# Optimization experiments

Measured on AMD Instinct MI355X. Metric: run time of the kernel, lower is better.

The kernel has to match this reference:

```python
import jax, jax.numpy as jnp
import numpy as np
import math

B, S, H, NH = 8, 1024, 1024, 16
DK = H // NH
EPS = 1e-6


def setup_inputs() -> dict:
    key = jax.random.key(0)
    ks = jax.random.split(key, 8)
    enc = jax.random.normal(ks[0], (B, S, H), dtype=jnp.float32)
    mask = jax.random.randint(ks[1], (B, 1, S, S), 0, 2, dtype=jnp.int32)
    scale = 1.0 / math.sqrt(H)
    W_Q = jax.random.normal(ks[2], (H, H), dtype=jnp.float32) * scale
    W_K = jax.random.normal(ks[3], (H, H), dtype=jnp.float32) * scale
    W_V = jax.random.normal(ks[4], (H, H), dtype=jnp.float32) * scale
    W_O = jax.random.normal(ks[5], (H, H), dtype=jnp.float32) * scale
    ln_gamma = jnp.ones((H,), dtype=jnp.float32)
    ln_beta = jnp.zeros((H,), dtype=jnp.float32)
    return {"enc": enc, "mask": mask, "W_Q": W_Q, "W_K": W_K, "W_V": W_V,
            "W_O": W_O, "ln_gamma": ln_gamma, "ln_beta": ln_beta}


def _layer_norm(x, gamma, beta):
    mu = jnp.mean(x, axis=-1, keepdims=True)
    var = jnp.mean(jnp.square(x - mu), axis=-1, keepdims=True)
    return (x - mu) / jnp.sqrt(var + EPS) * gamma + beta


def reference(enc, mask, W_Q, W_K, W_V, W_O, ln_gamma, ln_beta):
    # torch Linear: y = x @ W.T  (bias=False)
    # [B,S,H] -> [B,NH,S,DK]
    def heads(x, W):
        y = jnp.einsum('bsh,oh->bso', x, W)
        return y.reshape(B, S, NH, DK).transpose(0, 2, 1, 3)
    Q = heads(enc, W_Q)
    K = heads(enc, W_K)
    V = heads(enc, W_V)
    # attention scores [B,NH,S,S]
    scores = jnp.einsum('bhqd,bhkd->bhqk', Q, K) / math.sqrt(DK)
    scores = jnp.where(mask == 0, jnp.float32(-1e9), scores)
    attn_dist = jax.nn.softmax(scores, axis=-1)  # dropout_rate=0 -> no-op
    out = jnp.einsum('bhqk,bhkd->bhqd', attn_dist, V)
    out = out.transpose(0, 2, 1, 3).reshape(B, S, H)
    out = jnp.einsum('bsh,oh->bso', out, W_O)
    out = _layer_norm(out + enc, ln_gamma, ln_beta)
    return (out, attn_dist)
```

## Files before the change

### kernel.cpp

```cpp
#include <hip/hip_runtime.h>
#include <hip/hip_bf16.h>


typedef __bf16 bf16;
typedef __attribute__((ext_vector_type(8))) __bf16 bf16x8;
typedef __attribute__((ext_vector_type(4))) __bf16 bf16x4;
typedef __attribute__((ext_vector_type(4))) float f32x4;

#define MFMA16(a, b, c) __builtin_amdgcn_mfma_f32_16x16x32_bf16((a), (b), (c), 0, 0, 0)

#define B_ 8
#define S_ 1024
#define NH_ 16
#define DK_ 64
#define H_ 1024

__device__ __forceinline__ void gload_lds16b(const void* g, void* l) {
  __builtin_amdgcn_global_load_lds(
      (__attribute__((address_space(1))) void*)g,
      (__attribute__((address_space(3))) void*)l, 16, 0, 0);
}

__device__ __forceinline__ bf16x8 cat8(bf16x4 a, bf16x4 b) {
  bf16x8 r;
  r[0] = a[0]; r[1] = a[1]; r[2] = a[2]; r[3] = a[3];
  r[4] = b[0]; r[5] = b[1]; r[6] = b[2]; r[7] = b[3];
  return r;
}

__global__ __launch_bounds__(256) void cvt_all_kern(const float* __restrict__ enc,
                                                    const float* __restrict__ wq,
                                                    const float* __restrict__ wk,
                                                    const float* __restrict__ wv,
                                                    const float* __restrict__ wo_in,
                                                    const int* __restrict__ mask,
                                                    bf16* __restrict__ enc_bf,
                                                    bf16* __restrict__ wqkv,
                                                    bf16* __restrict__ wo,
                                                    unsigned char* __restrict__ mask8) {
  int i = blockIdx.x * 256 + threadIdx.x;
  if (i < 2097152) {
    float4 v = ((const float4*)enc)[i];
    bf16x4 o;
    o[0] = (bf16)v.x; o[1] = (bf16)v.y; o[2] = (bf16)v.z; o[3] = (bf16)v.w;
    ((bf16x4*)enc_bf)[i] = o;
  } else if (i < 3145728) {
    int j = i - 2097152;
    const float* src;
    bf16* dst;
    if (j < 262144) { src = wq; dst = (bf16*)wqkv; }
    else if (j < 524288) { src = wk; dst = wqkv + 1048576; j -= 262144; }
    else if (j < 786432) { src = wv; dst = wqkv + 2097152; j -= 524288; }
    else { src = wo_in; dst = wo; j -= 786432; }
    float4 v = ((const float4*)src)[j];
    bf16x4 o;
    o[0] = (bf16)v.x; o[1] = (bf16)v.y; o[2] = (bf16)v.z; o[3] = (bf16)v.w;
    ((bf16x4*)dst)[j] = o;
  } else {
    int j = i - 3145728;
    int4 v = ((const int4*)mask)[j];
    uchar4 o;
    o.x = (unsigned char)v.x; o.y = (unsigned char)v.y;
    o.z = (unsigned char)v.z; o.w = (unsigned char)v.w;
    ((uchar4*)mask8)[j] = o;
  }
}

template <bool F32OUT>
__global__ __launch_bounds__(256) void gemm_bt_kern(const bf16* __restrict__ A,
                                                    const bf16* __restrict__ Bt,
                                                    void* __restrict__ Cout,
                                                    const float* __restrict__ resid,
                                                    int K, int ldc) {
  __shared__ bf16 As[128 * 32];
  __shared__ bf16 Bs[128 * 32];
  const int lin = blockIdx.y * gridDim.x + blockIdx.x;
  const int nwg = gridDim.x * gridDim.y;
  const int chunk = nwg >> 3;
  const int v = (lin & 7) * chunk + (lin >> 3);
  const int m0 = (v / gridDim.x) * 128, n0 = (v % gridDim.x) * 128;
  const int tid = threadIdx.x;
  const int w = tid >> 6, l = tid & 63, l15 = l & 15, lg = l >> 4;
  const int wm = w >> 1, wn = w & 1;

  const bf16* Ab = A + (size_t)(m0 + (tid >> 2)) * K + (tid & 3) * 8;
  const bf16* Bb = Bt + (size_t)(n0 + (tid >> 2)) * K + (tid & 3) * 8;
  char* AsB = (char*)As + tid * 16;
  char* BsB = (char*)Bs + tid * 16;

  f32x4 acc[4][4] = {};
  for (int k0 = 0; k0 < K; k0 += 32) {
    gload_lds16b(Ab + k0, AsB);
    gload_lds16b(Ab + (size_t)64 * K + k0, AsB + 4096);
    gload_lds16b(Bb + k0, BsB);
    gload_lds16b(Bb + (size_t)64 * K + k0, BsB + 4096);
    __syncthreads();
    bf16x8 af[4], bfv[4];
#pragma unroll
    for (int m = 0; m < 4; m++)
      af[m] = *(const bf16x8*)&As[(wm * 64 + m * 16 + l15) * 32 + lg * 8];
#pragma unroll
    for (int n = 0; n < 4; n++)
      bfv[n] = *(const bf16x8*)&Bs[(wn * 64 + n * 16 + l15) * 32 + lg * 8];
#pragma unroll
    for (int m = 0; m < 4; m++)
#pragma unroll
      for (int n = 0; n < 4; n++) acc[m][n] = MFMA16(af[m], bfv[n], acc[m][n]);
    __syncthreads();
  }
#pragma unroll
  for (int m = 0; m < 4; m++)
#pragma unroll
    for (int n = 0; n < 4; n++)
#pragma unroll
      for (int j = 0; j < 4; j++) {
        int row = m0 + wm * 64 + m * 16 + lg * 4 + j;
        int col = n0 + wn * 64 + n * 16 + l15;
        if constexpr (F32OUT) {
          ((float*)Cout)[(size_t)row * ldc + col] =
              acc[m][n][j] + resid[(size_t)row * ldc + col];
        } else {
          ((bf16*)Cout)[(size_t)row * ldc + col] = (bf16)acc[m][n][j];
        }
      }
}

__global__ __launch_bounds__(256) void vtrans_kern(const bf16* __restrict__ qkv,
                                                   bf16* __restrict__ vT) {
  int blk = blockIdx.x;
  int st = blk & 15;
  int h = (blk >> 4) & 15;
  int b = blk >> 8;
  __shared__ bf16 t[64][65];
  int tid = threadIdx.x;
  {
    int r = tid >> 2, cb = (tid & 3) * 16;
    const bf16* src = qkv + ((size_t)(b * S_ + st * 64 + r)) * 3072 + 2048 + h * DK_ + cb;
    bf16x8 u0 = *(const bf16x8*)src;
    bf16x8 u1 = *(const bf16x8*)(src + 8);
#pragma unroll
    for (int j = 0; j < 8; j++) { t[r][cb + j] = u0[j]; t[r][cb + 8 + j] = u1[j]; }
  }
  __syncthreads();
  {
    int d = tid >> 2, sb = (tid & 3) * 16;
    bf16* dst = vT + ((size_t)((b * NH_ + h) * DK_ + d)) * S_ + st * 64 + sb;
#pragma unroll
    for (int j = 0; j < 16; j++) dst[j] = t[sb + j][d];
  }
}

#define PSTR 2056
#define MSTR 1032
#define KSTR 136

__global__ __launch_bounds__(512, 2) void attn_fused(const bf16* __restrict__ qkv,
                                                     const bf16* __restrict__ vT,
                                                     const unsigned char* __restrict__ mask8,
                                                     float* __restrict__ attn_out,
                                                     bf16* __restrict__ ctx) {
  __shared__ char smem[78848];
  char* Pb = smem;
  char* stg = smem + 65792;
  char* qtl = smem + 74496;
  float* red = (float*)(smem + 74496);

  const int vb = (blockIdx.x & 7) * 512 + (blockIdx.x >> 3);
  const int qt = vb & 31, h = (vb >> 5) & 15, b = vb >> 9;
  const int q0 = qt * 32;
  const int t = threadIdx.x;
  const int w = t >> 6, l = t & 63, l15 = l & 15, lg = l >> 4;
  const int qsub = w >> 2, ksub = w & 3;
  const int qrow = qsub * 16 + l15;

  const char* qkv_b = (const char*)qkv;
  const char* kb_g = qkv_b + (size_t)b * S_ * 6144 + 2048 + (size_t)h * 128;
  const char* vT_b = (const char*)vT + (size_t)(b * NH_ + h) * 64 * 2048;
  const unsigned char* mrow = mask8 + (size_t)b * S_ * S_ + (size_t)q0 * S_;

  const int srow = t >> 3, scol = (t & 7) * 16;

  uint4 qreg, mreg[4], kr0, kr1;
  if (t < 256) {
    int row = t >> 3;
    qreg = *(const uint4*)(qkv_b + (size_t)(b * S_ + q0 + row) * 6144 + h * 128 + scol);
  }
#pragma unroll
  for (int p = 0; p < 4; p++) {
    int row = (t >> 6) + p * 8, col = (t & 63) * 16;
    mreg[p] = *(const uint4*)(mrow + (size_t)row * 1024 + col);
  }
  kr0 = *(const uint4*)(kb_g + (size_t)srow * 6144 + scol);
  kr1 = *(const uint4*)(kb_g + (size_t)(64 + srow) * 6144 + scol);

  if (t < 256) {
    int row = t >> 3;
    *(uint2*)(qtl + row * KSTR + scol) = make_uint2(qreg.x, qreg.y);
    *(uint2*)(qtl + row * KSTR + scol + 8) = make_uint2(qreg.z, qreg.w);
  }
#pragma unroll
  for (int p = 0; p < 4; p++) {
    int row = (t >> 6) + p * 8, col = (t & 63) * 16;
    *(uint2*)(Pb + row * MSTR + col) = make_uint2(mreg[p].x, mreg[p].y);
    *(uint2*)(Pb + row * MSTR + col + 8) = make_uint2(mreg[p].z, mreg[p].w);
  }
  *(uint2*)(stg + srow * KSTR + scol) = make_uint2(kr0.x, kr0.y);
  *(uint2*)(stg + srow * KSTR + scol + 8) = make_uint2(kr0.z, kr0.w);
  __syncthreads();

  bf16x8 aq[2];
#pragma unroll
  for (int kk = 0; kk < 2; kk++) {
    bf16x4 a0 = *(bf16x4*)(qtl + qrow * KSTR + kk * 64 + lg * 16);
    bf16x4 a1 = *(bf16x4*)(qtl + qrow * KSTR + kk * 64 + lg * 16 + 8);
    aq[kk] = cat8(a0, a1);
  }

  f32x4 sc[16];
#pragma unroll
  for (int i = 0; i < 16; i++) sc[i] = (f32x4){0.f, 0.f, 0.f, 0.f};
  uint4 kr[2];
  kr[1] = kr1;
  const int krow = ksub * 16 + l15;
#pragma unroll
  for (int cc = 0; cc < 16; cc++) {
    if (cc < 14)
      kr[cc & 1] = *(const uint4*)(kb_g + (size_t)((cc + 2) * 64 + srow) * 6144 + scol);
#pragma unroll
    for (int kk = 0; kk < 2; kk++) {
      bf16x4 b0 = *(bf16x4*)(stg + krow * KSTR + kk * 64 + lg * 16);
      bf16x4 b1 = *(bf16x4*)(stg + krow * KSTR + kk * 64 + lg * 16 + 8);
      sc[cc] = MFMA16(cat8(b0, b1), aq[kk], sc[cc]);
    }
    __syncthreads();
    if (cc < 15) {
      uint4 kw = kr[(cc + 1) & 1];
      *(uint2*)(stg + srow * KSTR + scol) = make_uint2(kw.x, kw.y);
      *(uint2*)(stg + srow * KSTR + scol + 8) = make_uint2(kw.z, kw.w);
    }
    __syncthreads();
  }

  const float SCL = 0.125f * 1.44269504f;
  float rmax = -3e38f;
#pragma unroll
  for (int cc = 0; cc < 16; cc++) {
    int kb4 = cc * 64 + ksub * 16 + lg * 4;
    uchar4 mv = *(const uchar4*)(Pb + qrow * MSTR + kb4);
    unsigned char mb[4] = {mv.x, mv.y, mv.z, mv.w};
#pragma unroll
    for (int j = 0; j < 4; j++) {
      float s = sc[cc][j] * SCL;
      if (mb[j] == 0) s = -1e9f;
      sc[cc][j] = s;
      rmax = fmaxf(rmax, s);
    }
  }
  rmax = fmaxf(rmax, __shfl_xor(rmax, 16));
  rmax = fmaxf(rmax, __shfl_xor(rmax, 32));
  float rsum = 0.f;
#pragma unroll
  for (int cc = 0; cc < 16; cc++)
#pragma unroll
    for (int j = 0; j < 4; j++) {
      float e = exp2f(sc[cc][j] - rmax);
      sc[cc][j] = e;
      rsum += e;
    }
  rsum += __shfl_xor(rsum, 16);
  rsum += __shfl_xor(rsum, 32);
  if (lg == 0) {
    red[(w * 32 + qrow) * 2] = rmax;
    red[(w * 32 + qrow) * 2 + 1] = rsum;
  }
  __syncthreads();
  float gm = -3e38f, gs = 0.f;
  const int g4 = qsub * 4;
#pragma unroll
  for (int i = 0; i < 4; i++) gm = fmaxf(gm, red[((g4 + i) * 32 + qrow) * 2]);
#pragma unroll
  for (int i = 0; i < 4; i++)
    gs += red[((g4 + i) * 32 + qrow) * 2 + 1] * exp2f(red[((g4 + i) * 32 + qrow) * 2] - gm);
  const float scale = exp2f(rmax - gm) / gs;

#pragma unroll
  for (int cc = 0; cc < 16; cc++) {
    bf16x4 pb;
#pragma unroll
    for (int j = 0; j < 4; j++) pb[j] = (bf16)(sc[cc][j] * scale);
    *(bf16x4*)(Pb + qrow * PSTR + cc * 128 + ksub * 32 + lg * 8) = pb;
  }
  uint4 vr[2];
  vr[0] = *(const uint4*)(vT_b + (size_t)srow * 2048 + scol);
  vr[1] = *(const uint4*)(vT_b + (size_t)srow * 2048 + 128 + scol);
  __syncthreads();
  *(uint2*)(stg + srow * KSTR + scol) = make_uint2(vr[0].x, vr[0].y);
  *(uint2*)(stg + srow * KSTR + scol + 8) = make_uint2(vr[0].z, vr[0].w);

  {
    int row = t >> 4, c16 = t & 15;
    float* arow = attn_out + (size_t)((b * NH_ + h) * S_ + q0 + row) * S_;
#pragma unroll
    for (int it = 0; it < 16; it++) {
      bf16x4 pv = *(bf16x4*)(Pb + row * PSTR + c16 * 8 + it * 128);
      f32x4 o4;
#pragma unroll
      for (int j = 0; j < 4; j++) o4[j] = (float)pv[j];
      __builtin_nontemporal_store(o4, (f32x4*)(arow + c16 * 4 + it * 64));
    }
  }
  __syncthreads();

  f32x4 o = {0.f, 0.f, 0.f, 0.f};
  const int dkr = ksub * 16 + l15;
#pragma unroll
  for (int cc = 0; cc < 16; cc++) {
    if (cc < 14)
      vr[cc & 1] = *(const uint4*)(vT_b + (size_t)srow * 2048 + (cc + 2) * 128 + scol);
#pragma unroll
    for (int tt = 0; tt < 2; tt++) {
      bf16x4 p0 = *(bf16x4*)(Pb + qrow * PSTR + cc * 128 + tt * 64 + lg * 16);
      bf16x4 p1 = *(bf16x4*)(Pb + qrow * PSTR + cc * 128 + tt * 64 + lg * 16 + 8);
      bf16x4 v0 = *(bf16x4*)(stg + dkr * KSTR + tt * 64 + lg * 16);
      bf16x4 v1 = *(bf16x4*)(stg + dkr * KSTR + tt * 64 + lg * 16 + 8);
      o = MFMA16(cat8(p0, p1), cat8(v0, v1), o);
    }
    __syncthreads();
    if (cc < 15) {
      uint4 vw = vr[(cc + 1) & 1];
      *(uint2*)(stg + srow * KSTR + scol) = make_uint2(vw.x, vw.y);
      *(uint2*)(stg + srow * KSTR + scol + 8) = make_uint2(vw.z, vw.w);
    }
    __syncthreads();
  }

#pragma unroll
  for (int jj = 0; jj < 4; jj++) {
    int row = qsub * 16 + lg * 4 + jj;
    *(bf16*)(stg + row * KSTR + (ksub * 16 + l15) * 2) = (bf16)o[jj];
  }
  __syncthreads();
  if (t < 256) {
    int row = t >> 3;
    bf16x4 c0 = *(bf16x4*)(stg + row * KSTR + scol);
    bf16x4 c1 = *(bf16x4*)(stg + row * KSTR + scol + 8);
    bf16x8 cv = cat8(c0, c1);
    *(bf16x8*)((char*)ctx + (size_t)(b * S_ + q0 + row) * 2048 + h * 128 + scol) = cv;
  }
}

__global__ __launch_bounds__(256) void ln_kern(float* __restrict__ y,
                                               const float* __restrict__ gamma,
                                               const float* __restrict__ beta) {
  int row = blockIdx.x;
  int tid = threadIdx.x;
  float4 v = *(const float4*)&y[(size_t)row * 1024 + tid * 4];
  float s = v.x + v.y + v.z + v.w;
  float q = v.x * v.x + v.y * v.y + v.z * v.z + v.w * v.w;
#pragma unroll
  for (int m = 1; m < 64; m <<= 1) { s += __shfl_xor(s, m); q += __shfl_xor(q, m); }
  __shared__ float rb[8];
  if ((tid & 63) == 0) { rb[(tid >> 6) * 2] = s; rb[(tid >> 6) * 2 + 1] = q; }
  __syncthreads();
  s = rb[0] + rb[2] + rb[4] + rb[6];
  q = rb[1] + rb[3] + rb[5] + rb[7];
  float mu = s * (1.f / 1024.f);
  float var = q * (1.f / 1024.f) - mu * mu;
  float rstd = rsqrtf(var + 1e-6f);
  float4 g = *(const float4*)&gamma[tid * 4];
  float4 bb = *(const float4*)&beta[tid * 4];
  float4 o;
  o.x = (v.x - mu) * rstd * g.x + bb.x;
  o.y = (v.y - mu) * rstd * g.y + bb.y;
  o.z = (v.z - mu) * rstd * g.z + bb.z;
  o.w = (v.w - mu) * rstd * g.w + bb.w;
  *(float4*)&y[(size_t)row * 1024 + tid * 4] = o;
}

extern "C" void kernel_launch(void* const* d_in, const int* in_sizes, int n_in,
                              void* d_out, int out_size, void* d_ws, size_t ws_size,
                              hipStream_t stream) {
  const float* enc = (const float*)d_in[0];
  const int* mask = (const int*)d_in[1];
  const float* W_Q = (const float*)d_in[2];
  const float* W_K = (const float*)d_in[3];
  const float* W_V = (const float*)d_in[4];
  const float* W_O = (const float*)d_in[5];
  const float* ln_g = (const float*)d_in[6];
  const float* ln_b = (const float*)d_in[7];

  float* out_f32 = (float*)d_out;
  float* attn_f32 = (float*)d_out + (size_t)B_ * S_ * H_;

  char* wsb = (char*)d_ws;
  bf16* enc_bf = (bf16*)wsb;
  bf16* wqkv = (bf16*)(wsb + 16777216);
  bf16* wo = (bf16*)(wsb + 23068672);
  bf16* qkv = (bf16*)(wsb + 25165824);
  bf16* vT = (bf16*)(wsb + 75497472);
  bf16* ctx = (bf16*)(wsb + 92274688);
  unsigned char* mask8 = (unsigned char*)(wsb + 109051904);

  cvt_all_kern<<<20480, 256, 0, stream>>>(enc, W_Q, W_K, W_V, W_O, mask,
                                          enc_bf, wqkv, wo, mask8);

  gemm_bt_kern<false><<<dim3(24, 64), 256, 0, stream>>>(enc_bf, wqkv, qkv, nullptr, 1024, 3072);

  vtrans_kern<<<2048, 256, 0, stream>>>(qkv, vT);

  attn_fused<<<4096, 512, 0, stream>>>(qkv, vT, mask8, attn_f32, ctx);

  gemm_bt_kern<true><<<dim3(8, 64), 256, 0, stream>>>(ctx, wo, out_f32, enc, 1024, 1024);

  ln_kern<<<8192, 256, 0, stream>>>(out_f32, ln_g, ln_b);
}
```

Before: 296.9 us.

## Use 256x256 double-buffered GEMM kernel for QKV projection

Adds a new 512-thread GEMM kernel with 256x256 output tiles, 128-wide K steps, XOR-swizzled LDS layout and double-buffered direct global-to-LDS loads. The QKV projection now uses it in place of the 128x128 kernel. The larger tile raises data reuse per load and overlaps the next stage's loads with MFMA work. In exchange it uses 128KB of LDS per block, gives only 384 blocks on the GPU, and writes output with scalar bf16 stores.

```diff
diff --git a/kernel.cpp b/kernel.cpp
--- a/kernel.cpp
+++ b/kernel.cpp
@@ -66,6 +66,96 @@
   }
 }
 
+__global__ __launch_bounds__(512, 2) void gemm256_kern(const bf16* __restrict__ A,
+                                                       const bf16* __restrict__ Bt,
+                                                       bf16* __restrict__ C,
+                                                       int N, int NT) {
+  __shared__ char Ab[2][32768];
+  __shared__ char Bb[2][32768];
+  const int nwg = gridDim.x;
+  const int chunk = nwg >> 3;
+  const int lin = blockIdx.x;
+  const int v = (lin & 7) * chunk + (lin >> 3);
+  const int tm = v / NT, tn = v % NT;
+  const size_t m0 = (size_t)tm * 256, n0 = (size_t)tn * 256;
+  const int t = threadIdx.x;
+  const int l = t & 63, l15 = l & 15, lg = l >> 4;
+  const int w = t >> 6, wr = w >> 2, wc = w & 3;
+
+  const int row_t = t >> 3;
+  const int scol = (((t & 7) ^ (row_t & 7)) << 4);
+  const size_t Kb = 2048;
+  const char* Ag = (const char*)A + (m0 + row_t) * Kb + scol;
+  const char* Bg = (const char*)Bt + (n0 + row_t) * Kb + scol;
+  const int dst = t * 16;
+
+#define STAGE256(kt, buf)                                                      \
+  {                                                                            \
+    const size_t ko = (size_t)(kt) * 128;                                      \
+    _Pragma("unroll") for (int ld = 0; ld < 4; ld++)                           \
+        gload_lds16b(Ag + (size_t)ld * 64 * Kb + ko, &Ab[buf][ld * 8192 + dst]); \
+    _Pragma("unroll") for (int ld = 0; ld < 4; ld++)                           \
+        gload_lds16b(Bg + (size_t)ld * 64 * Kb + ko, &Bb[buf][ld * 8192 + dst]); \
+  }
+
+  const int sw = (l15 & 7) << 4;
+  const int arowb = wr * 16384 + l15 * 128;
+  const int browb = wc * 8192 + l15 * 128;
+
+  f32x4 acc[8][4] = {};
+
+  STAGE256(0, 0);
+  STAGE256(1, 1);
+  asm volatile("s_waitcnt vmcnt(8)" ::: "memory");
+  __builtin_amdgcn_sched_barrier(0);
+  __builtin_amdgcn_s_barrier();
+
+  for (int it = 0; it < 16; ++it) {
+    const int buf = it & 1;
+#pragma unroll
+    for (int kk = 0; kk < 2; kk++) {
+      bf16x8 a[8], b[4];
+#pragma unroll
+      for (int i = 0; i < 8; i++)
+        a[i] = *(const bf16x8*)&Ab[buf][arowb + i * 2048 + ((kk * 64 + lg * 16) ^ sw)];
+#pragma unroll
+      for (int n = 0; n < 4; n++)
+        b[n] = *(const bf16x8*)&Bb[buf][browb + n * 2048 + ((kk * 64 + lg * 16) ^ sw)];
+      __builtin_amdgcn_s_setprio(1);
+#pragma unroll
+      for (int i = 0; i < 8; i++)
+#pragma unroll
+        for (int n = 0; n < 4; n++) acc[i][n] = MFMA16(a[i], b[n], acc[i][n]);
+      __builtin_amdgcn_s_setprio(0);
+    }
+    asm volatile("s_waitcnt lgkmcnt(0)" ::: "memory");
+    __builtin_amdgcn_sched_barrier(0);
+    __builtin_amdgcn_s_barrier();
+    if (it < 14) STAGE256(it + 2, buf);
+    if (it < 15) {
+      if (it == 14) {
+        asm volatile("s_waitcnt vmcnt(0)" ::: "memory");
+      } else {
+        asm volatile("s_waitcnt vmcnt(8)" ::: "memory");
+      }
+      __builtin_amdgcn_sched_barrier(0);
+      __builtin_amdgcn_s_barrier();
+    }
+  }
+
+#pragma unroll
+  for (int i = 0; i < 8; i++)
+#pragma unroll
+    for (int n = 0; n < 4; n++)
+#pragma unroll
+      for (int j = 0; j < 4; j++) {
+        size_t row = m0 + wr * 128 + i * 16 + lg * 4 + j;
+        size_t col = n0 + wc * 64 + n * 16 + l15;
+        C[row * (size_t)N + col] = (bf16)acc[i][n][j];
+      }
+#undef STAGE256
+}
+
 template <bool F32OUT>
 __global__ __launch_bounds__(256) void gemm_bt_kern(const bf16* __restrict__ A,
                                                     const bf16* __restrict__ Bt,
@@ -404,7 +494,7 @@
   cvt_all_kern<<<20480, 256, 0, stream>>>(enc, W_Q, W_K, W_V, W_O, mask,
                                           enc_bf, wqkv, wo, mask8);
 
-  gemm_bt_kern<false><<<dim3(24, 64), 256, 0, stream>>>(enc_bf, wqkv, qkv, nullptr, 1024, 3072);
+  gemm256_kern<<<384, 512, 0, stream>>>(enc_bf, wqkv, qkv, 3072, 12);
 
   vtrans_kern<<<2048, 256, 0, stream>>>(qkv, vT);
 
```

New measurement: 298.6 us. About the same (+0.6%).

## Double-buffer K/V LDS staging with XOR-swizzled layout and single barrier per step

Applied to the files above, without the earlier changes.

The attention kernel now double-buffers the K and V staging tiles in LDS, so each pipeline step needs one barrier instead of two. The staging and P tiles switch from padded strides to XOR-swizzled 128/2048-byte rows, which allows full 16-byte LDS reads and writes without bank conflicts. Barriers use a custom macro that waits on lgkmcnt and pins the schedule. LDS use grows slightly (82KB vs 79KB), which could affect the two-blocks-per-CU occupancy target.

```diff
diff --git a/kernel.cpp b/kernel.cpp
--- a/kernel.cpp
+++ b/kernel.cpp
@@ -14,6 +14,14 @@
 #define NH_ 16
 #define DK_ 64
 #define H_ 1024
+
+#define SBAR()                                         \
+  {                                                    \
+    asm volatile("s_waitcnt lgkmcnt(0)" ::: "memory"); \
+    __builtin_amdgcn_sched_barrier(0);                 \
+    __builtin_amdgcn_s_barrier();                      \
+    __builtin_amdgcn_sched_barrier(0);                 \
+  }
 
 __device__ __forceinline__ void gload_lds16b(const void* g, void* l) {
   __builtin_amdgcn_global_load_lds(
@@ -150,20 +158,19 @@
   }
 }
 
-#define PSTR 2056
 #define MSTR 1032
-#define KSTR 136
-
-__global__ __launch_bounds__(512, 2) void attn_fused(const bf16* __restrict__ qkv,
-                                                     const bf16* __restrict__ vT,
-                                                     const unsigned char* __restrict__ mask8,
-                                                     float* __restrict__ attn_out,
-                                                     bf16* __restrict__ ctx) {
-  __shared__ char smem[78848];
+
+__global__ __launch_bounds__(512, 2) void attn_db(const bf16* __restrict__ qkv,
+                                                  const bf16* __restrict__ vT,
+                                                  const unsigned char* __restrict__ mask8,
+                                                  float* __restrict__ attn_out,
+                                                  bf16* __restrict__ ctx) {
+  __shared__ char smem[81920];
   char* Pb = smem;
-  char* stg = smem + 65792;
-  char* qtl = smem + 74496;
-  float* red = (float*)(smem + 74496);
+  char* mk = smem;
+  char* qtl = smem + 36864;
+  float* red = (float*)(smem + 41216);
+  char* stg = smem + 65536;
 
   const int vb = (blockIdx.x & 7) * 512 + (blockIdx.x >> 3);
   const int qt = vb & 31, h = (vb >> 5) & 15, b = vb >> 9;
@@ -172,47 +179,48 @@
   const int w = t >> 6, l = t & 63, l15 = l & 15, lg = l >> 4;
   const int qsub = w >> 2, ksub = w & 3;
   const int qrow = qsub * 16 + l15;
+  const int psw = (qrow & 7) << 4;
 
   const char* qkv_b = (const char*)qkv;
   const char* kb_g = qkv_b + (size_t)b * S_ * 6144 + 2048 + (size_t)h * 128;
   const char* vT_b = (const char*)vT + (size_t)(b * NH_ + h) * 64 * 2048;
   const unsigned char* mrow = mask8 + (size_t)b * S_ * S_ + (size_t)q0 * S_;
 
-  const int srow = t >> 3, scol = (t & 7) * 16;
+  const int srow = t >> 3, sslot = t & 7;
+  const int swz_w = srow * 128 + ((sslot ^ (srow & 7)) << 4);
 
   uint4 qreg, mreg[4], kr0, kr1;
   if (t < 256) {
     int row = t >> 3;
-    qreg = *(const uint4*)(qkv_b + (size_t)(b * S_ + q0 + row) * 6144 + h * 128 + scol);
+    qreg = *(const uint4*)(qkv_b + (size_t)(b * S_ + q0 + row) * 6144 + h * 128 + sslot * 16);
   }
 #pragma unroll
   for (int p = 0; p < 4; p++) {
     int row = (t >> 6) + p * 8, col = (t & 63) * 16;
     mreg[p] = *(const uint4*)(mrow + (size_t)row * 1024 + col);
   }
-  kr0 = *(const uint4*)(kb_g + (size_t)srow * 6144 + scol);
-  kr1 = *(const uint4*)(kb_g + (size_t)(64 + srow) * 6144 + scol);
+  kr0 = *(const uint4*)(kb_g + (size_t)srow * 6144 + sslot * 16);
+  kr1 = *(const uint4*)(kb_g + (size_t)(64 + srow) * 6144 + sslot * 16);
 
   if (t < 256) {
-    int row = t >> 3;
-    *(uint2*)(qtl + row * KSTR + scol) = make_uint2(qreg.x, qreg.y);
-    *(uint2*)(qtl + row * KSTR + scol + 8) = make_uint2(qreg.z, qreg.w);
+    int row = t >> 3, c = sslot * 16;
+    *(uint2*)(qtl + row * 136 + c) = make_uint2(qreg.x, qreg.y);
+    *(uint2*)(qtl + row * 136 + c + 8) = make_uint2(qreg.z, qreg.w);
   }
 #pragma unroll
   for (int p = 0; p < 4; p++) {
     int row = (t >> 6) + p * 8, col = (t & 63) * 16;
-    *(uint2*)(Pb + row * MSTR + col) = make_uint2(mreg[p].x, mreg[p].y);
-    *(uint2*)(Pb + row * MSTR + col + 8) = make_uint2(mreg[p].z, mreg[p].w);
-  }
-  *(uint2*)(stg + srow * KSTR + scol) = make_uint2(kr0.x, kr0.y);
-  *(uint2*)(stg + srow * KSTR + scol + 8) = make_uint2(kr0.z, kr0.w);
+    *(uint2*)(mk + row * MSTR + col) = make_uint2(mreg[p].x, mreg[p].y);
+    *(uint2*)(mk + row * MSTR + col + 8) = make_uint2(mreg[p].z, mreg[p].w);
+  }
+  *(uint4*)(stg + swz_w) = kr0;
   __syncthreads();
 
   bf16x8 aq[2];
 #pragma unroll
   for (int kk = 0; kk < 2; kk++) {
-    bf16x4 a0 = *(bf16x4*)(qtl + qrow * KSTR + kk * 64 + lg * 16);
-    bf16x4 a1 = *(bf16x4*)(qtl + qrow * KSTR + kk * 64 + lg * 16 + 8);
+    bf16x4 a0 = *(bf16x4*)(qtl + qrow * 136 + kk * 64 + lg * 16);
+    bf16x4 a1 = *(bf16x4*)(qtl + qrow * 136 + kk * 64 + lg * 16 + 8);
     aq[kk] = cat8(a0, a1);
   }
 
@@ -224,21 +232,19 @@
   const int krow = ksub * 16 + l15;
 #pragma unroll
   for (int cc = 0; cc < 16; cc++) {
+    const int cur = cc & 1;
+#pragma unroll
+    for (int kk = 0; kk < 2; kk++) {
+      const int slot = (kk * 4 + lg) ^ (krow & 7);
+      bf16x8 kf = *(const bf16x8*)(stg + cur * 8192 + krow * 128 + slot * 16);
+      sc[cc] = MFMA16(kf, aq[kk], sc[cc]);
+    }
     if (cc < 14)
-      kr[cc & 1] = *(const uint4*)(kb_g + (size_t)((cc + 2) * 64 + srow) * 6144 + scol);
-#pragma unroll
-    for (int kk = 0; kk < 2; kk++) {
-      bf16x4 b0 = *(bf16x4*)(stg + krow * KSTR + kk * 64 + lg * 16);
-      bf16x4 b1 = *(bf16x4*)(stg + krow * KSTR + kk * 64 + lg * 16 + 8);
-      sc[cc] = MFMA16(cat8(b0, b1), aq[kk], sc[cc]);
-    }
-    __syncthreads();
+      kr[cc & 1] = *(const uint4*)(kb_g + (size_t)((cc + 2) * 64 + srow) * 6144 + sslot * 16);
     if (cc < 15) {
-      uint4 kw = kr[(cc + 1) & 1];
-      *(uint2*)(stg + srow * KSTR + scol) = make_uint2(kw.x, kw.y);
-      *(uint2*)(stg + srow * KSTR + scol + 8) = make_uint2(kw.z, kw.w);
-    }
-    __syncthreads();
+      *(uint4*)(stg + (cur ^ 1) * 8192 + swz_w) = kr[(cc + 1) & 1];
+      SBAR();
+    }
   }
 
   const float SCL = 0.125f * 1.44269504f;
@@ -246,7 +252,7 @@
 #pragma unroll
   for (int cc = 0; cc < 16; cc++) {
     int kb4 = cc * 64 + ksub * 16 + lg * 4;
-    uchar4 mv = *(const uchar4*)(Pb + qrow * MSTR + kb4);
+    uchar4 mv = *(const uchar4*)(mk + qrow * MSTR + kb4);
     unsigned char mb[4] = {mv.x, mv.y, mv.z, mv.w};
 #pragma unroll
     for (int j = 0; j < 4; j++) {
@@ -273,7 +279,7 @@
     red[(w * 32 + qrow) * 2] = rmax;
     red[(w * 32 + qrow) * 2 + 1] = rsum;
   }
-  __syncthreads();
+  SBAR();
   float gm = -3e38f, gs = 0.f;
   const int g4 = qsub * 4;
 #pragma unroll
@@ -282,70 +288,69 @@
   for (int i = 0; i < 4; i++)
     gs += red[((g4 + i) * 32 + qrow) * 2 + 1] * exp2f(red[((g4 + i) * 32 + qrow) * 2] - gm);
   const float scale = exp2f(rmax - gm) / gs;
-
+  SBAR();
+
+  uint4 vr[2];
+  vr[0] = *(const uint4*)(vT_b + (size_t)srow * 2048 + sslot * 16);
+  vr[1] = *(const uint4*)(vT_b + (size_t)srow * 2048 + 128 + sslot * 16);
 #pragma unroll
   for (int cc = 0; cc < 16; cc++) {
     bf16x4 pb;
 #pragma unroll
     for (int j = 0; j < 4; j++) pb[j] = (bf16)(sc[cc][j] * scale);
-    *(bf16x4*)(Pb + qrow * PSTR + cc * 128 + ksub * 32 + lg * 8) = pb;
-  }
-  uint4 vr[2];
-  vr[0] = *(const uint4*)(vT_b + (size_t)srow * 2048 + scol);
-  vr[1] = *(const uint4*)(vT_b + (size_t)srow * 2048 + 128 + scol);
-  __syncthreads();
-  *(uint2*)(stg + srow * KSTR + scol) = make_uint2(vr[0].x, vr[0].y);
-  *(uint2*)(stg + srow * KSTR + scol + 8) = make_uint2(vr[0].z, vr[0].w);
+    *(bf16x4*)(Pb + qrow * 2048 + ((cc * 128 + ksub * 32 + lg * 8) ^ psw)) = pb;
+  }
+  SBAR();
+  *(uint4*)(stg + swz_w) = vr[0];
 
   {
     int row = t >> 4, c16 = t & 15;
+    int rsw = (row & 7) << 4;
     float* arow = attn_out + (size_t)((b * NH_ + h) * S_ + q0 + row) * S_;
 #pragma unroll
     for (int it = 0; it < 16; it++) {
-      bf16x4 pv = *(bf16x4*)(Pb + row * PSTR + c16 * 8 + it * 128);
+      bf16x4 pv = *(bf16x4*)(Pb + row * 2048 + ((c16 * 8 + it * 128) ^ rsw));
       f32x4 o4;
 #pragma unroll
       for (int j = 0; j < 4; j++) o4[j] = (float)pv[j];
       __builtin_nontemporal_store(o4, (f32x4*)(arow + c16 * 4 + it * 64));
     }
   }
-  __syncthreads();
+  SBAR();
 
   f32x4 o = {0.f, 0.f, 0.f, 0.f};
   const int dkr = ksub * 16 + l15;
 #pragma unroll
   for (int cc = 0; cc < 16; cc++) {
+    const int cur = cc & 1;
+#pragma unroll
+    for (int tt = 0; tt < 2; tt++) {
+      const int slot = (tt * 4 + lg) ^ (dkr & 7);
+      bf16x8 vf = *(const bf16x8*)(stg + cur * 8192 + dkr * 128 + slot * 16);
+      bf16x8 pf = *(const bf16x8*)(Pb + qrow * 2048 + ((cc * 128 + tt * 64 + lg * 16) ^ psw));
+      o = MFMA16(pf, vf, o);
+    }
     if (cc < 14)
-      vr[cc & 1] = *(const uint4*)(vT_b + (size_t)srow * 2048 + (cc + 2) * 128 + scol);
-#pragma unroll
-    for (int tt = 0; tt < 2; tt++) {
-      bf16x4 p0 = *(bf16x4*)(Pb + qrow * PSTR + cc * 128 + tt * 64 + lg * 16);
-      bf16x4 p1 = *(bf16x4*)(Pb + qrow * PSTR + cc * 128 + tt * 64 + lg * 16 + 8);
-      bf16x4 v0 = *(bf16x4*)(stg + dkr * KSTR + tt * 64 + lg * 16);
-      bf16x4 v1 = *(bf16x4*)(stg + dkr * KSTR + tt * 64 + lg * 16 + 8);
-      o = MFMA16(cat8(p0, p1), cat8(v0, v1), o);
-    }
-    __syncthreads();
+      vr[cc & 1] = *(const uint4*)(vT_b + (size_t)srow * 2048 + (cc + 2) * 128 + sslot * 16);
     if (cc < 15) {
-      uint4 vw = vr[(cc + 1) & 1];
-      *(uint2*)(stg + srow * KSTR + scol) = make_uint2(vw.x, vw.y);
-      *(uint2*)(stg + srow * KSTR + scol + 8) = make_uint2(vw.z, vw.w);
-    }
-    __syncthreads();
-  }
+      *(uint4*)(stg + (cur ^ 1) * 8192 + swz_w) = vr[(cc + 1) & 1];
+      SBAR();
+    }
+  }
+  SBAR();
 
 #pragma unroll
   for (int jj = 0; jj < 4; jj++) {
     int row = qsub * 16 + lg * 4 + jj;
-    *(bf16*)(stg + row * KSTR + (ksub * 16 + l15) * 2) = (bf16)o[jj];
-  }
-  __syncthreads();
+    *(bf16*)(stg + row * 136 + (ksub * 16 + l15) * 2) = (bf16)o[jj];
+  }
+  SBAR();
   if (t < 256) {
-    int row = t >> 3;
-    bf16x4 c0 = *(bf16x4*)(stg + row * KSTR + scol);
-    bf16x4 c1 = *(bf16x4*)(stg + row * KSTR + scol + 8);
+    int row = t >> 3, c = sslot * 16;
+    bf16x4 c0 = *(bf16x4*)(stg + row * 136 + c);
+    bf16x4 c1 = *(bf16x4*)(stg + row * 136 + c + 8);
     bf16x8 cv = cat8(c0, c1);
-    *(bf16x8*)((char*)ctx + (size_t)(b * S_ + q0 + row) * 2048 + h * 128 + scol) = cv;
+    *(bf16x8*)((char*)ctx + (size_t)(b * S_ + q0 + row) * 2048 + h * 128 + c) = cv;
   }
 }
 
@@ -408,7 +413,7 @@
 
   vtrans_kern<<<2048, 256, 0, stream>>>(qkv, vT);
 
-  attn_fused<<<4096, 512, 0, stream>>>(qkv, vT, mask8, attn_f32, ctx);
+  attn_db<<<4096, 512, 0, stream>>>(qkv, vT, mask8, attn_f32, ctx);
 
   gemm_bt_kern<true><<<dim3(8, 64), 256, 0, stream>>>(ctx, wo, out_f32, enc, 1024, 1024);
 
```

Result: slower. 320.9 us (+8.1%).

## Add triple-buffered 8-wave QKV GEMM with direct-to-LDS loads and swizzle

Applied to the files above, without the earlier changes.

Replaces the QKV projection GEMM with a new kernel using 128x256 tiles, 512 threads and K-tiles of 64. A/B tiles are loaded straight into LDS through a three-stage ring buffer with XOR-swizzled columns, and the loads are spread across MFMA phases with manual waitcnt, barriers and priority settings. The aim is to hide global-load latency and avoid LDS bank conflicts in the largest GEMM. In exchange it uses 144KB of LDS for one block per CU, and its hard-coded sizes and fine-grained synchronisation are fragile.

```diff
diff --git a/kernel.cpp b/kernel.cpp
--- a/kernel.cpp
+++ b/kernel.cpp
@@ -66,6 +66,117 @@
   }
 }
 
+__global__ __launch_bounds__(512, 1) void gemm8p_kern(const bf16* __restrict__ A,
+                                                      const bf16* __restrict__ Bt,
+                                                      bf16* __restrict__ C) {
+  __shared__ char Ab[3][16384];
+  __shared__ char Bb[3][32768];
+  const int lin = blockIdx.x;
+  const int v = (lin & 7) * 96 + (lin >> 3);
+  const size_t m0 = (size_t)(v / 12) * 128, n0 = (size_t)(v % 12) * 256;
+  const int t = threadIdx.x;
+  const int l = t & 63, l15 = l & 15, lg = l >> 4;
+  const int w = t >> 6, wr = w >> 2, wc = w & 3;
+
+  const int row_t = t >> 3;
+  const int scol = (((t & 7) ^ (row_t & 7)) << 4);
+  const char* Ag = (const char*)A + (m0 + row_t) * 2048 + scol;
+  const char* Bg = (const char*)Bt + (n0 + row_t) * 2048 + scol;
+  const int dst16 = t * 16;
+  const int sw = (l15 & 7) << 4;
+
+#define STAGE_A(kt, bp)                                      \
+  {                                                          \
+    const size_t ko = (size_t)(kt) * 128;                    \
+    gload_lds16b(Ag + ko, &Ab[bp][dst16]);                   \
+    gload_lds16b(Ag + 131072 + ko, &Ab[bp][8192 + dst16]);   \
+  }
+#define STAGE_B01(kt, bp)                                    \
+  {                                                          \
+    const size_t ko = (size_t)(kt) * 128;                    \
+    gload_lds16b(Bg + ko, &Bb[bp][dst16]);                   \
+    gload_lds16b(Bg + 131072 + ko, &Bb[bp][8192 + dst16]);   \
+  }
+#define STAGE_B23(kt, bp)                                    \
+  {                                                          \
+    const size_t ko = (size_t)(kt) * 128;                    \
+    gload_lds16b(Bg + 262144 + ko, &Bb[bp][16384 + dst16]);  \
+    gload_lds16b(Bg + 393216 + ko, &Bb[bp][24576 + dst16]);  \
+  }
+
+  f32x4 acc[4][4] = {};
+
+  STAGE_A(0, 0); STAGE_B01(0, 0); STAGE_B23(0, 0);
+  STAGE_A(1, 1); STAGE_B01(1, 1); STAGE_B23(1, 1);
+  asm volatile("s_waitcnt vmcnt(6)" ::: "memory");
+  __builtin_amdgcn_sched_barrier(0);
+  __builtin_amdgcn_s_barrier();
+
+  int buf = 0;
+  for (int kt = 0; kt < 16; ++kt) {
+    const int nb = (buf + 2 >= 3) ? buf - 1 : buf + 2;
+    const char* Ac = Ab[buf];
+    const char* Bc = Bb[buf];
+#pragma unroll
+    for (int p = 0; p < 4; ++p) {
+      const int pr = p >> 1, pc = p & 1;
+      bf16x8 af[2][2], bfv[2][2];
+#pragma unroll
+      for (int i = 0; i < 2; i++)
+#pragma unroll
+        for (int kk = 0; kk < 2; kk++) {
+          const int ar = wr * 64 + pr * 32 + i * 16 + l15;
+          af[i][kk] = *(const bf16x8*)&Ac[ar * 128 + ((kk * 64 + lg * 16) ^ sw)];
+          const int br = wc * 64 + pc * 32 + i * 16 + l15;
+          bfv[i][kk] = *(const bf16x8*)&Bc[br * 128 + ((kk * 64 + lg * 16) ^ sw)];
+        }
+      if (kt < 14) {
+        if (p == 0) STAGE_A(kt + 2, nb)
+        else if (p == 1) STAGE_B01(kt + 2, nb)
+        else if (p == 2) STAGE_B23(kt + 2, nb)
+      }
+      __builtin_amdgcn_s_barrier();
+      asm volatile("s_waitcnt lgkmcnt(0)" ::: "memory");
+      __builtin_amdgcn_sched_barrier(0);
+      __builtin_amdgcn_s_setprio(1);
+#pragma unroll
+      for (int i = 0; i < 2; i++)
+#pragma unroll
+        for (int n = 0; n < 2; n++)
+#pragma unroll
+          for (int kk = 0; kk < 2; kk++)
+            acc[pr * 2 + i][pc * 2 + n] =
+                MFMA16(af[i][kk], bfv[n][kk], acc[pr * 2 + i][pc * 2 + n]);
+      __builtin_amdgcn_s_setprio(0);
+      __builtin_amdgcn_s_barrier();
+    }
+    if (kt < 15) {
+      if (kt == 14) {
+        asm volatile("s_waitcnt vmcnt(0)" ::: "memory");
+      } else {
+        asm volatile("s_waitcnt vmcnt(6)" ::: "memory");
+      }
+      __builtin_amdgcn_sched_barrier(0);
+      __builtin_amdgcn_s_barrier();
+    }
+    buf = (buf + 1 == 3) ? 0 : buf + 1;
+  }
+#undef STAGE_A
+#undef STAGE_B01
+#undef STAGE_B23
+
+#pragma unroll
+  for (int i2 = 0; i2 < 4; i2++)
+#pragma unroll
+    for (int n2 = 0; n2 < 4; n2++)
+#pragma unroll
+      for (int j = 0; j < 4; j++) {
+        size_t row = m0 + wr * 64 + i2 * 16 + lg * 4 + j;
+        size_t col = n0 + wc * 64 + n2 * 16 + l15;
+        C[row * 3072 + col] = (bf16)acc[i2][n2][j];
+      }
+}
+
 template <bool F32OUT>
 __global__ __launch_bounds__(256) void gemm_bt_kern(const bf16* __restrict__ A,
                                                     const bf16* __restrict__ Bt,
@@ -404,7 +515,7 @@
   cvt_all_kern<<<20480, 256, 0, stream>>>(enc, W_Q, W_K, W_V, W_O, mask,
                                           enc_bf, wqkv, wo, mask8);
 
-  gemm_bt_kern<false><<<dim3(24, 64), 256, 0, stream>>>(enc_bf, wqkv, qkv, nullptr, 1024, 3072);
+  gemm8p_kern<<<768, 512, 0, stream>>>(enc_bf, wqkv, qkv);
 
   vtrans_kern<<<2048, 256, 0, stream>>>(qkv, vT);
 
```

Result: slower. 313.9 us (+5.7%).
